# Performance work log

Hardware: AMD Instinct MI355X
Metric: run time of the kernel (lower is better)

Reference implementation:

```python
import jax, jax.numpy as jnp
import numpy as np

B, LATENT, H, OUT, T, L = 4096, 128, 256, 88, 64, 5  # batch, latent, hidden, output(88 keys), seq_len, num_layers


def setup_inputs() -> dict:
    key = jax.random.key(0)
    ks = jax.random.split(key, 8)
    sc = 1.0 / np.sqrt(H)
    n = lambda k, shp, s: (jax.random.normal(k, shp, jnp.float32) * s)
    return {
        "x": jax.random.normal(ks[0], (B, LATENT), jnp.float32),
        "linear_w": n(ks[1], (H, LATENT), 1.0 / np.sqrt(LATENT)),
        "linear_b": jnp.zeros((H,), jnp.float32),
        # PyTorch LSTM layout: [4H, in] with gate order i, f, g, o. Layer-0 input size == H.
        "w_ih": n(ks[2], (L, 4 * H, H), sc),
        "w_hh": n(ks[3], (L, 4 * H, H), sc),
        "b_ih": n(ks[4], (L, 4 * H), sc),
        "b_hh": n(ks[5], (L, 4 * H), sc),
        "out_w": n(ks[6], (OUT, H), sc),
        "out_b": jnp.zeros((OUT,), jnp.float32),
    }


def _lstm_cell(gates, c):
    # gates: [B, 4H] pre-activation, PyTorch order i, f, g, o
    i, f, g, o = jnp.split(gates, 4, axis=-1)
    c_new = jax.nn.sigmoid(f) * c + jax.nn.sigmoid(i) * jnp.tanh(g)
    h_new = jax.nn.sigmoid(o) * jnp.tanh(c_new)
    return h_new, c_new


def _lstm(xp, w_ih, w_hh, b_ih, b_hh):
    # xp: [B, H] latent projection, repeated over T timesteps (constant input).
    bsz = xp.shape[0]
    gx0 = xp @ w_ih[0].T + b_ih[0]  # layer-0 input gates, constant across time [B, 4H]
    h0 = jnp.zeros((L, bsz, H), xp.dtype)
    c0 = jnp.zeros((L, bsz, H), xp.dtype)

    def step(carry, _):
        h, c = carry  # [L, B, H]
        hs, cs = [], []
        layer_in_gates = gx0
        for l in range(L):  # fixed small loop over structurally distinct layers
            if l > 0:
                layer_in_gates = hs[-1] @ w_ih[l].T + b_ih[l]
            gates = layer_in_gates + h[l] @ w_hh[l].T + b_hh[l]
            hl, cl = _lstm_cell(gates, c[l])
            hs.append(hl)
            cs.append(cl)
        return (jnp.stack(hs), jnp.stack(cs)), hs[-1]

    _, ys = jax.lax.scan(step, (h0, c0), None, length=T)  # ys: [T, B, H]
    return ys.transpose(1, 0, 2)  # [B, T, H]


def reference(x, linear_w, linear_b, w_ih, w_hh, b_ih, b_hh, out_w, out_b):
    xp = x @ linear_w.T + linear_b  # [B, H]; unsqueeze+repeat folded into constant gx0
    y = _lstm(xp, w_ih, w_hh, b_ih, b_hh)  # [B, T, H]
    return jax.nn.sigmoid(y @ out_w.T + out_b)  # [B, T, OUT]
```

## Files before the change

kernel.cpp:

```cpp
#include <hip/hip_runtime.h>
#include <hip/hip_bf16.h>
#include <cstdint>

#define B_ 4096
#define H_ 256
#define G_ 1024
#define T_ 64
#define L_ 5

typedef __hip_bfloat16 bf16;
typedef __bf16 bf16x8 __attribute__((ext_vector_type(8)));
typedef float f32x4 __attribute__((ext_vector_type(4)));

#define OFF_WCOMB   0ull
#define OFF_WIH0R   5242880ull
#define OFF_LWB     5767168ull
#define OFF_XB      5832704ull
#define OFF_OBW     6881280ull
#define OFF_BIAS    6930432ull
#define OFF_XP      6950912ull
#define OFF_GX0     9048064ull
#define OFF_H0      25825280ull
#define OFF_H1      34213888ull
#define OFF_C1      42602496ull
#define OFF_YS      63574016ull
#define OFF_C0      199888896ull
#define TOTAL_WS    220860416ull
#define SLOT_H      2097152ull
#define SLOT_C      4194304ull

__device__ __forceinline__ bf16* h_ptr(char* ws, int l, int p) {
  return (bf16*)(ws + (p ? OFF_H1 : OFF_H0) + (size_t)l * SLOT_H);
}
__device__ __forceinline__ float* c_ptr(char* ws, int l, int p) {
  return (float*)(ws + (p ? OFF_C1 : OFF_C0) + (size_t)l * SLOT_C);
}
__device__ __forceinline__ bf16* ys_ptr(char* ws, int s) {
  return (bf16*)(ws + OFF_YS + (size_t)s * SLOT_H);
}

__device__ __forceinline__ float frcp(float x) { return __builtin_amdgcn_rcpf(x); }
__device__ __forceinline__ float fsig(float x) { return frcp(1.0f + __expf(-x)); }
__device__ __forceinline__ float ftanh(float x) { return 1.0f - 2.0f * frcp(1.0f + __expf(2.0f * x)); }

__device__ __forceinline__ void gload16(const void* g, void* l) {
  __builtin_amdgcn_global_load_lds((const __attribute__((address_space(1))) void*)g,
                                   (__attribute__((address_space(3))) void*)l, 16, 0, 0);
}

__device__ __forceinline__ void stage_tile(char* dst, const bf16* src, long stride, int koff,
                                           int wv, int lane) {
#pragma unroll
  for (int i = 0; i < 4; ++i) {
    int r = 32 * wv + 8 * i + (lane >> 3);
    int cb = ((lane & 7) << 4) ^ ((r & 7) << 4);
    const bf16* g = src + (long)r * stride + koff + (cb >> 1);
    char* ld = dst + (32 * wv + 8 * i) * 128;
    gload16(g, ld);
  }
}

template <int OUTMODE>
__device__ void gemm_core(const bf16* __restrict__ A1, int lda1,
                          const bf16* __restrict__ A2,
                          const bf16* __restrict__ W, int ldw, int K,
                          const float* __restrict__ bias,
                          const float* __restrict__ acc2d,
                          float* __restrict__ outF, bf16* __restrict__ outB, int ldo,
                          const float* __restrict__ cIn, float* __restrict__ cOut,
                          bf16* __restrict__ hOut,
                          int mtile, int ntile, char* smem) {
  const int tid = threadIdx.x;
  const int lane = tid & 63, wv = tid >> 6;
  const int wrow = wv >> 1, wcol = wv & 1;
  const int row0 = mtile * 128;
  const int n0 = ntile * 128;

  char* As = smem;
  char* Bs = smem + 16384;

  f32x4 acc[4][4];
  if (acc2d) {
#pragma unroll
    for (int m = 0; m < 4; m++)
#pragma unroll
      for (int n = 0; n < 4; n++)
#pragma unroll
        for (int r = 0; r < 4; r++) {
          int row = row0 + wrow * 64 + 16 * m + ((lane >> 4) << 2) + r;
          int col = n0 + wcol * 64 + 16 * n + (lane & 15);
          acc[m][n][r] = acc2d[(long)row * G_ + col];
        }
  } else {
#pragma unroll
    for (int n = 0; n < 4; n++) {
      int col = n0 + wcol * 64 + 16 * n + (lane & 15);
      float bv = bias ? bias[col] : 0.0f;
#pragma unroll
      for (int m = 0; m < 4; m++)
#pragma unroll
        for (int r = 0; r < 4; r++) acc[m][n][r] = bv;
    }
  }

  const int nkb = K >> 6;
  for (int kb = 0; kb < nkb; ++kb) {
    if (kb < 4) stage_tile(As, A1 + (long)row0 * lda1, lda1, kb * 64, wv, lane);
    else        stage_tile(As, A2 + (long)row0 * 256,  256,  kb * 64 - 256, wv, lane);
    stage_tile(Bs, W + (long)n0 * ldw, ldw, kb * 64, wv, lane);
    __syncthreads();
#pragma unroll
    for (int ks = 0; ks < 2; ++ks) {
      bf16x8 af[4], bfr[4];
#pragma unroll
      for (int m = 0; m < 4; m++) {
        int r = wrow * 64 + 16 * m + (lane & 15);
        int cb = (ks * 64 + ((lane >> 4) << 4)) ^ ((r & 7) << 4);
        af[m] = *(const bf16x8*)(As + r * 128 + cb);
      }
#pragma unroll
      for (int n = 0; n < 4; n++) {
        int r = wcol * 64 + 16 * n + (lane & 15);
        int cb = (ks * 64 + ((lane >> 4) << 4)) ^ ((r & 7) << 4);
        bfr[n] = *(const bf16x8*)(Bs + r * 128 + cb);
      }
#pragma unroll
      for (int m = 0; m < 4; m++)
#pragma unroll
        for (int n = 0; n < 4; n++)
          acc[m][n] = __builtin_amdgcn_mfma_f32_16x16x32_bf16(af[m], bfr[n], acc[m][n], 0, 0, 0);
    }
    __syncthreads();
  }

  if (OUTMODE == 0 || OUTMODE == 1) {
#pragma unroll
    for (int m = 0; m < 4; m++)
#pragma unroll
      for (int n = 0; n < 4; n++)
#pragma unroll
        for (int r = 0; r < 4; r++) {
          int row = row0 + wrow * 64 + 16 * m + ((lane >> 4) << 2) + r;
          int col = n0 + wcol * 64 + 16 * n + (lane & 15);
          if (OUTMODE == 0) outF[(long)row * ldo + col] = acc[m][n][r];
          else              outB[(long)row * ldo + col] = __float2bfloat16(acc[m][n][r]);
        }
  } else {
#pragma unroll
    for (int h = 0; h < 2; ++h) {
      if (wcol == h) {
#pragma unroll
        for (int m = 0; m < 4; m++)
#pragma unroll
          for (int n = 0; n < 4; n++)
#pragma unroll
            for (int r = 0; r < 4; r++) {
              int rr = wrow * 64 + 16 * m + ((lane >> 4) << 2) + r;
              int cc2 = 16 * n + (lane & 15);
              *(float*)(smem + rr * 256 + ((cc2 << 2) ^ ((rr & 7) << 4))) = acc[m][n][r];
            }
      }
      __syncthreads();
      int j2 = tid & 15;
      int rb = tid >> 4;
#pragma unroll
      for (int i = 0; i < 8; i++) {
        int rr = rb + 16 * i;
        f32x4 g4 = *(const f32x4*)(smem + rr * 256 + ((j2 << 4) ^ ((rr & 7) << 4)));
        int row = row0 + rr;
        int jj = ntile * 32 + 16 * h + j2;
        float cold = cIn ? cIn[(long)row * H_ + jj] : 0.0f;
        float cn = fsig(g4[1]) * cold + fsig(g4[0]) * ftanh(g4[2]);
        float hn = fsig(g4[3]) * ftanh(cn);
        cOut[(long)row * H_ + jj] = cn;
        hOut[(long)row * H_ + jj] = __float2bfloat16(hn);
      }
      if (h == 0) __syncthreads();
    }
  }
}

template <int OUTMODE>
__global__ __launch_bounds__(256) void gemm_generic(const bf16* A1, int lda1,
                                                    const bf16* W, int ldw, int K,
                                                    const float* bias,
                                                    float* outF, bf16* outB, int ldo) {
  __shared__ __align__(16) char smem[32768];
  int mtile = blockIdx.x & 31;
  int ntile = blockIdx.x >> 5;
  gemm_core<OUTMODE>(A1, lda1, A1 , W, ldw, K, bias, nullptr,
                     outF, outB, ldo, nullptr, nullptr, nullptr, mtile, ntile, smem);
}

__global__ __launch_bounds__(256) void lstm_diag(int d, char* __restrict__ ws) {
  __shared__ __align__(16) char smem[32768];
  int l0 = d > 63 ? d - 63 : 0;
  int l = l0 + blockIdx.y;
  int t = d - l;
  int bid = blockIdx.x;
  int wg = (bid & 7) * 32 + (bid >> 3);
  int w = wg & 31, q = wg >> 5;
  int mtile = q * 4 + (w & 3);
  int ntile = w >> 2;
  int sp = (t & 1) ^ 1, op = t & 1;
  bool tz = (t == 0);

  const bf16* wc = (const bf16*)(ws + OFF_WCOMB) + (long)l * G_ * 512;
  const bf16* A1; const bf16* A2; int K;
  const float* bias = nullptr; const float* acc2d = nullptr;
  if (l == 0) {
    A1 = h_ptr(ws, 0, sp); A2 = A1;
    K = tz ? 0 : 256;
    acc2d = (const float*)(ws + OFF_GX0);
  } else {
    A1 = h_ptr(ws, l - 1, op);
    A2 = (l == 4) ? ys_ptr(ws, t) : h_ptr(ws, l, sp);
    K = tz ? 256 : 512;
    bias = (const float*)(ws + OFF_BIAS) + l * G_;
  }
  const float* cIn = tz ? nullptr : c_ptr(ws, l, sp);
  float* cOut = c_ptr(ws, l, op);
  bf16* hOut = (l == 4) ? ys_ptr(ws, t + 1) : h_ptr(ws, l, op);

  gemm_core<2>(A1, 256, A2, wc, 512, K, bias, acc2d,
               nullptr, nullptr, 0, cIn, cOut, hOut, mtile, ntile, smem);
}

__global__ __launch_bounds__(256) void proj_kernel(char* __restrict__ ws,
                                                   const float* __restrict__ ob,
                                                   float* __restrict__ out) {
  __shared__ __align__(16) char smem[49152];
  int mtile = blockIdx.x;
  int t = blockIdx.y;
  const bf16* ys = ys_ptr(ws, t + 1);
  const char* obw = (const char*)(ws + OFF_OBW);
  int tid = threadIdx.x, lane = tid & 63, wv = tid >> 6;
#pragma unroll
  for (int i = 0; i < 12; i++) {
    int r = wv * 24 + i * 2 + (lane >> 5);
    int cb = ((lane & 31) << 4) ^ ((r & 7) << 4);
    gload16(obw + r * 512 + cb, smem + (wv * 24 + i * 2) * 512);
  }
  __syncthreads();
  f32x4 acc[2][6];
#pragma unroll
  for (int m = 0; m < 2; m++)
#pragma unroll
    for (int n = 0; n < 6; n++)
#pragma unroll
      for (int r = 0; r < 4; r++) acc[m][n][r] = 0.0f;
  const char* arow = (const char*)(ys + (long)(mtile * 128) * 256);
  for (int kk = 0; kk < 256; kk += 32) {
    bf16x8 af[2], bfr[6];
#pragma unroll
    for (int m = 0; m < 2; m++) {
      int r = wv * 32 + 16 * m + (lane & 15);
      af[m] = *(const bf16x8*)(arow + (long)r * 512 + kk * 2 + ((lane >> 4) << 4));
    }
#pragma unroll
    for (int n = 0; n < 6; n++) {
      int r = 16 * n + (lane & 15);
      int cb = (kk * 2 + ((lane >> 4) << 4)) ^ ((r & 7) << 4);
      bfr[n] = *(const bf16x8*)(smem + r * 512 + cb);
    }
#pragma unroll
    for (int m = 0; m < 2; m++)
#pragma unroll
      for (int n = 0; n < 6; n++)
        acc[m][n] = __builtin_amdgcn_mfma_f32_16x16x32_bf16(af[m], bfr[n], acc[m][n], 0, 0, 0);
  }
#pragma unroll
  for (int m = 0; m < 2; m++)
#pragma unroll
    for (int n = 0; n < 6; n++)
#pragma unroll
      for (int r = 0; r < 4; r++) {
        int row = mtile * 128 + wv * 32 + 16 * m + ((lane >> 4) << 2) + r;
        int o = 16 * n + (lane & 15);
        if (o < 88) {
          float v = acc[m][n][r] + ob[o];
          out[((long)row * T_ + t) * 88 + o] = fsig(v);
        }
      }
}

__global__ void prep_kernel(const float* __restrict__ x, const float* __restrict__ lw,
                            const float* __restrict__ wih, const float* __restrict__ whh,
                            const float* __restrict__ bih, const float* __restrict__ bhh,
                            const float* __restrict__ ow, char* __restrict__ ws) {
  bf16* xb = (bf16*)(ws + OFF_XB);
  bf16* lwb = (bf16*)(ws + OFF_LWB);
  bf16* wcomb = (bf16*)(ws + OFF_WCOMB);
  bf16* wih0r = (bf16*)(ws + OFF_WIH0R);
  bf16* obw = (bf16*)(ws + OFF_OBW);
  float* bias = (float*)(ws + OFF_BIAS);
  const int S0 = 524288, S1 = 32768, S2 = 2621440, S3 = 262144, S4 = 24576, S5 = 5120;
  const int total = S0 + S1 + S2 + S3 + S4 + S5;
  for (int i = blockIdx.x * blockDim.x + threadIdx.x; i < total; i += gridDim.x * blockDim.x) {
    int idx = i;
    if (idx < S0) { xb[idx] = __float2bfloat16(x[idx]); continue; }
    idx -= S0;
    if (idx < S1) { lwb[idx] = __float2bfloat16(lw[idx]); continue; }
    idx -= S1;
    if (idx < S2) {
      int l = idx >> 19;
      int rem = idx & 524287;
      int n = rem >> 9;
      int k = rem & 511;
      int row = (n & 3) * 256 + (n >> 2);
      float v;
      if (l == 0) v = (k < 256) ? whh[row * 256 + k] : 0.0f;
      else        v = (k < 256) ? wih[(l * 1024 + row) * 256 + k]
                                : whh[(l * 1024 + row) * 256 + (k - 256)];
      wcomb[idx] = __float2bfloat16(v); continue;
    }
    idx -= S2;
    if (idx < S3) {
      int n = idx >> 8, k = idx & 255;
      int row = (n & 3) * 256 + (n >> 2);
      wih0r[idx] = __float2bfloat16(wih[row * 256 + k]); continue;
    }
    idx -= S3;
    if (idx < S4) {
      int r = idx >> 8, k = idx & 255;
      obw[idx] = __float2bfloat16(r < 88 ? ow[r * 256 + k] : 0.0f); continue;
    }
    idx -= S4;
    {
      int l = idx >> 10, n = idx & 1023;
      int row = (n & 3) * 256 + (n >> 2);
      bias[idx] = bih[l * 1024 + row] + bhh[l * 1024 + row];
    }
  }
}

extern "C" void kernel_launch(void* const* d_in, const int* in_sizes, int n_in,
                              void* d_out, int out_size, void* d_ws, size_t ws_size,
                              hipStream_t stream) {
  const float* x   = (const float*)d_in[0];
  const float* lw  = (const float*)d_in[1];
  const float* lb  = (const float*)d_in[2];
  const float* wih = (const float*)d_in[3];
  const float* whh = (const float*)d_in[4];
  const float* bih = (const float*)d_in[5];
  const float* bhh = (const float*)d_in[6];
  const float* ow  = (const float*)d_in[7];
  const float* ob  = (const float*)d_in[8];
  char* ws = (char*)d_ws;
  float* out = (float*)d_out;

  if (ws_size < TOTAL_WS) return;

  prep_kernel<<<2048, 256, 0, stream>>>(x, lw, wih, whh, bih, bhh, ow, ws);

  gemm_generic<1><<<dim3(64), 256, 0, stream>>>(
      (const bf16*)(ws + OFF_XB), 128, (const bf16*)(ws + OFF_LWB), 128, 128,
      lb, nullptr, (bf16*)(ws + OFF_XP), 256);

  gemm_generic<0><<<dim3(256), 256, 0, stream>>>(
      (const bf16*)(ws + OFF_XP), 256, (const bf16*)(ws + OFF_WIH0R), 256, 256,
      (const float*)(ws + OFF_BIAS), (float*)(ws + OFF_GX0), nullptr, 1024);

  for (int d = 0; d < 68; ++d) {
    int lo = d > 63 ? d - 63 : 0;
    int hi = d < 4 ? d : 4;
    int nc = hi - lo + 1;
    lstm_diag<<<dim3(256, nc), 256, 0, stream>>>(d, ws);
  }

  proj_kernel<<<dim3(32, 64), 256, 0, stream>>>(ws, ob, out);
}
```

Measured before the change: 2.987 ms.

## Fold latent projection into layer-0 input weights; simplify LSTM tile mapping

Precomputes W_ih0·W_lin as one combined weight, plus a folded bias, so the layer-0 input gates come from a single K=128 GEMM on x instead of two chained GEMMs. The LSTM diagonal kernel drops its swizzled block-to-tile mapping for a plain linear one, and launch_bounds now request 3 blocks per SU. The weight fold adds a small extra GEMM and a serial bias kernel, and it changes bf16 rounding because the product is formed before quantizing. The mapping change may alter cache locality across blocks within a diagonal.

```diff
diff --git a/kernel.cpp b/kernel.cpp
--- a/kernel.cpp
+++ b/kernel.cpp
@@ -14,11 +14,12 @@
 
 #define OFF_WCOMB   0ull
 #define OFF_WIH0R   5242880ull
-#define OFF_LWB     5767168ull
+#define OFF_LWT     5767168ull
 #define OFF_XB      5832704ull
 #define OFF_OBW     6881280ull
 #define OFF_BIAS    6930432ull
-#define OFF_XP      6950912ull
+#define OFF_W1      6950912ull
+#define OFF_B0X     7213056ull
 #define OFF_GX0     9048064ull
 #define OFF_H0      25825280ull
 #define OFF_H1      34213888ull
@@ -181,10 +182,10 @@
 }
 
 template <int OUTMODE>
-__global__ __launch_bounds__(256) void gemm_generic(const bf16* A1, int lda1,
-                                                    const bf16* W, int ldw, int K,
-                                                    const float* bias,
-                                                    float* outF, bf16* outB, int ldo) {
+__global__ __launch_bounds__(256, 3) void gemm_generic(const bf16* A1, int lda1,
+                                                       const bf16* W, int ldw, int K,
+                                                       const float* bias,
+                                                       float* outF, bf16* outB, int ldo) {
   __shared__ __align__(16) char smem[32768];
   int mtile = blockIdx.x & 31;
   int ntile = blockIdx.x >> 5;
@@ -192,16 +193,13 @@
                      outF, outB, ldo, nullptr, nullptr, nullptr, mtile, ntile, smem);
 }
 
-__global__ __launch_bounds__(256) void lstm_diag(int d, char* __restrict__ ws) {
+__global__ __launch_bounds__(256, 3) void lstm_diag(int d, char* __restrict__ ws) {
   __shared__ __align__(16) char smem[32768];
   int l0 = d > 63 ? d - 63 : 0;
   int l = l0 + blockIdx.y;
   int t = d - l;
-  int bid = blockIdx.x;
-  int wg = (bid & 7) * 32 + (bid >> 3);
-  int w = wg & 31, q = wg >> 5;
-  int mtile = q * 4 + (w & 3);
-  int ntile = w >> 2;
+  int mtile = blockIdx.x & 31;
+  int ntile = blockIdx.x >> 5;
   int sp = (t & 1) ^ 1, op = t & 1;
   bool tz = (t == 0);
 
@@ -289,7 +287,7 @@
                             const float* __restrict__ bih, const float* __restrict__ bhh,
                             const float* __restrict__ ow, char* __restrict__ ws) {
   bf16* xb = (bf16*)(ws + OFF_XB);
-  bf16* lwb = (bf16*)(ws + OFF_LWB);
+  bf16* lwt = (bf16*)(ws + OFF_LWT);
   bf16* wcomb = (bf16*)(ws + OFF_WCOMB);
   bf16* wih0r = (bf16*)(ws + OFF_WIH0R);
   bf16* obw = (bf16*)(ws + OFF_OBW);
@@ -300,7 +298,10 @@
     int idx = i;
     if (idx < S0) { xb[idx] = __float2bfloat16(x[idx]); continue; }
     idx -= S0;
-    if (idx < S1) { lwb[idx] = __float2bfloat16(lw[idx]); continue; }
+    if (idx < S1) {
+      int r = idx >> 8, c = idx & 255;
+      lwt[idx] = __float2bfloat16(lw[c * 128 + r]); continue;
+    }
     idx -= S1;
     if (idx < S2) {
       int l = idx >> 19;
@@ -332,6 +333,16 @@
       bias[idx] = bih[l * 1024 + row] + bhh[l * 1024 + row];
     }
   }
+}
+
+__global__ void bias_fix_kernel(const float* __restrict__ lb, char* __restrict__ ws) {
+  int n = blockIdx.x * blockDim.x + threadIdx.x;
+  if (n >= 1024) return;
+  const bf16* wih0r = (const bf16*)(ws + OFF_WIH0R) + (long)n * 256;
+  const float* biasS = (const float*)(ws + OFF_BIAS);
+  float s = biasS[n];
+  for (int k = 0; k < 256; ++k) s += __bfloat162float(wih0r[k]) * lb[k];
+  ((float*)(ws + OFF_B0X))[n] = s;
 }
 
 extern "C" void kernel_launch(void* const* d_in, const int* in_sizes, int n_in,
@@ -353,13 +364,15 @@
 
   prep_kernel<<<2048, 256, 0, stream>>>(x, lw, wih, whh, bih, bhh, ow, ws);
 
-  gemm_generic<1><<<dim3(64), 256, 0, stream>>>(
-      (const bf16*)(ws + OFF_XB), 128, (const bf16*)(ws + OFF_LWB), 128, 128,
-      lb, nullptr, (bf16*)(ws + OFF_XP), 256);
+  gemm_generic<1><<<dim3(8), 256, 0, stream>>>(
+      (const bf16*)(ws + OFF_WIH0R), 256, (const bf16*)(ws + OFF_LWT), 256, 256,
+      nullptr, nullptr, (bf16*)(ws + OFF_W1), 128);
+
+  bias_fix_kernel<<<4, 256, 0, stream>>>(lb, ws);
 
   gemm_generic<0><<<dim3(256), 256, 0, stream>>>(
-      (const bf16*)(ws + OFF_XP), 256, (const bf16*)(ws + OFF_WIH0R), 256, 256,
-      (const float*)(ws + OFF_BIAS), (float*)(ws + OFF_GX0), nullptr, 1024);
+      (const bf16*)(ws + OFF_XB), 128, (const bf16*)(ws + OFF_W1), 128, 128,
+      (const float*)(ws + OFF_B0X), (float*)(ws + OFF_GX0), nullptr, 1024);
 
   for (int d = 0; d < 68; ++d) {
     int lo = d > 63 ? d - 63 : 0;
```

Result: faster. 2.578 ms (-13.7%).
